# Optimization experiments

Measured on AMD Instinct MI355X. Metric: run time of the kernel, lower is better.

Reference implementation:

```python
import jax, jax.numpy as jnp
import numpy as np

H = 8          # num heads
DK = 64        # d_model // H
D_MODEL = 512
WIN = 256


def setup_inputs() -> dict:
    key = jax.random.key(0)
    ks = jax.random.split(key, 12)
    B, S = 2, 2048
    mk = lambda k, shape, s=1.0: jax.random.normal(k, shape, dtype=jnp.float32) * s
    inp = {
        "query": mk(ks[0], (B, S, D_MODEL)),
        "key_in": mk(ks[1], (B, S, D_MODEL)),
        "value": mk(ks[2], (B, S, D_MODEL)),
        # nn.Linear(d_model, d_model) weights (out,in) and biases, x4
        "Wq": mk(ks[3], (D_MODEL, D_MODEL), 0.02), "bq": jnp.zeros((D_MODEL,), jnp.float32),
        "Wk": mk(ks[4], (D_MODEL, D_MODEL), 0.02), "bk": jnp.zeros((D_MODEL,), jnp.float32),
        "Wv": mk(ks[5], (D_MODEL, D_MODEL), 0.02), "bv": jnp.zeros((D_MODEL,), jnp.float32),
        "Wo": mk(ks[6], (D_MODEL, D_MODEL), 0.02), "bo": jnp.zeros((D_MODEL,), jnp.float32),
    }
    return inp


def reference(query, key_in, value, Wq, bq, Wk, bk, Wv, bv, Wo, bo):
    B, S, D = query.shape
    scale = np.float32(1.0 / np.sqrt(DK))

    def proj(x, W, b):
        # (B,S,D) -> (B,H,S,DK)
        return (x @ W.T + b).reshape(B, S, H, DK).transpose(0, 2, 1, 3)

    q = proj(query, Wq, bq)
    k = proj(key_in, Wk, bk)
    v = proj(value, Wv, bv)

    # Faithful to naive_masked_matmul: full (B,H,S,S) scores, with entries
    # OUTSIDE the sliding window left at exactly 0.0 (NOT -inf) before softmax.
    scores = jnp.einsum('bhid,bhjd->bhij', q, k) * scale
    idx = jnp.arange(S)
    band = jnp.abs(idx[:, None] - idx[None, :]) <= (WIN // 2)  # (S,S) bool
    scores = jnp.where(band, scores, jnp.float32(0.0))

    p_attn = jax.nn.softmax(scores, axis=-1)
    x = jnp.einsum('bhij,bhjd->bhid', p_attn, v)          # (B,H,S,DK)
    x = x.transpose(0, 2, 1, 3).reshape(B, S, D)          # (B,S,D)
    return x @ Wo.T + bo
```

## Files before the change

kernel.cpp:

```cpp
#include <hip/hip_runtime.h>
#include <hip/hip_bf16.h>

#define SS 2048
#define DD 512
#define HWIN 128

typedef __bf16 bf16x8 __attribute__((ext_vector_type(8)));
typedef unsigned short u16x8 __attribute__((ext_vector_type(8)));
typedef float f32x4 __attribute__((ext_vector_type(4)));

__device__ __forceinline__ unsigned short f2bf(float x) {
    unsigned u = __builtin_bit_cast(unsigned, x);
    return (unsigned short)((u + 0x7fffu + ((u >> 16) & 1u)) >> 16);
}
__device__ __forceinline__ float bf2f(unsigned short s) {
    unsigned u = ((unsigned)s) << 16;
    return __builtin_bit_cast(float, u);
}
__device__ __forceinline__ void split_bf(float x, unsigned short& h, unsigned short& l) {
    h = f2bf(x);
    l = f2bf(x - bf2f(h));
}
__device__ __forceinline__ void split8(float4 f0, float4 f1, u16x8& h, u16x8& l) {
    const float vals[8] = {f0.x, f0.y, f0.z, f0.w, f1.x, f1.y, f1.z, f1.w};
    #pragma unroll
    for (int i = 0; i < 8; ++i) {
        unsigned short hh, ll;
        split_bf(vals[i], hh, ll);
        h[i] = hh;
        l[i] = ll;
    }
}
__device__ __forceinline__ f32x4 mfma16(u16x8 a, u16x8 b, f32x4 c) {
    return __builtin_amdgcn_mfma_f32_16x16x32_bf16(
        __builtin_bit_cast(bf16x8, a), __builtin_bit_cast(bf16x8, b), c, 0, 0, 0);
}
__device__ __forceinline__ void gload16(const unsigned short* g, unsigned short* l) {
    __builtin_amdgcn_global_load_lds(
        (const __attribute__((address_space(1))) unsigned int*)g,
        (__attribute__((address_space(3))) unsigned int*)l, 16, 0, 0);
}

__global__ __launch_bounds__(256) void castW(
    const float* __restrict__ wq, const float* __restrict__ wk,
    const float* __restrict__ wv, const float* __restrict__ wo,
    unsigned short* __restrict__ WP, unsigned short* __restrict__ WoP)
{
    const size_t e0 = ((size_t)blockIdx.x * 256 + threadIdx.x) * 8;
    const float* src; size_t off; unsigned short* dst;
    if      (e0 < 262144) { src = wq; off = e0;          dst = WP + 2 * e0; }
    else if (e0 < 524288) { src = wk; off = e0 - 262144; dst = WP + 2 * e0; }
    else if (e0 < 786432) { src = wv; off = e0 - 524288; dst = WP + 2 * e0; }
    else                  { src = wo; off = e0 - 786432; dst = WoP + 2 * (e0 - 786432); }
    u16x8 h, l;
    split8(*(const float4*)(src + off), *(const float4*)(src + off + 4), h, l);
    *(u16x8*)(dst)     = h;
    *(u16x8*)(dst + 8) = l;
}

__global__ __launch_bounds__(256) void proj_gemm(
    const float* __restrict__ q, const float* __restrict__ k, const float* __restrict__ v,
    const unsigned short* __restrict__ WP,
    const float* __restrict__ bq, const float* __restrict__ bk, const float* __restrict__ bv,
    unsigned short* __restrict__ base,
    unsigned short* __restrict__ VTH, unsigned short* __restrict__ VTL)
{
    const int d = blockIdx.x;
    const int hi = d >> 6, low = d & 63;
    const int x = low >> 3, rsw = low & 7;
    const int g = hi * 8 + rsw;
    const int y = g / 3, z = g - y * 3;

    const float* A = (z == 0) ? q : ((z == 1) ? k : v);
    const unsigned short* Wp = WP + (size_t)z * 524288;
    const float* bias = (z == 0) ? bq : ((z == 1) ? bk : bv);
    unsigned short* OH = base + (size_t)z * 4194304;
    unsigned short* OL = OH + 2097152;

    const int m0 = y * 128, n0 = x * 64;

    __shared__ unsigned short Ah[8 * 64 * 8], Al[8 * 64 * 8];
    __shared__ unsigned short Bh[4 * 64 * 8], Bl[4 * 64 * 8];

    const int tid = threadIdx.x, wave = tid >> 6, lane = tid & 63;
    const int lm = lane & 15, lq = lane >> 4;
    const int wm = wave >> 1, wn = wave & 1;
    const int kb = lq * 8;

    f32x4 acc[4][2] = {};

    const int ar0 = m0 + (wave * 2 + 0) * 16 + lm;
    const int ar1 = m0 + (wave * 2 + 1) * 16 + lm;
    const int br  = n0 + wave * 16 + lm;

    unsigned short* aD0h = &Ah[((wave * 2 + 0) * 64 + lane) * 8];
    unsigned short* aD1h = &Ah[((wave * 2 + 1) * 64 + lane) * 8];
    unsigned short* aD0l = &Al[((wave * 2 + 0) * 64 + lane) * 8];
    unsigned short* aD1l = &Al[((wave * 2 + 1) * 64 + lane) * 8];
    unsigned short* bDh  = &Bh[(wave * 64 + lane) * 8];
    unsigned short* bDl  = &Bl[(wave * 64 + lane) * 8];

    for (int k0 = 0; k0 < 512; k0 += 32) {
        const float* p0 = A + (size_t)ar0 * 512 + k0 + kb;
        const float4 f00 = *(const float4*)p0, f01 = *(const float4*)(p0 + 4);
        const float* p1 = A + (size_t)ar1 * 512 + k0 + kb;
        const float4 f10 = *(const float4*)p1, f11 = *(const float4*)(p1 + 4);

        __syncthreads();
        u16x8 a0h, a0l, a1h, a1l;
        split8(f00, f01, a0h, a0l);
        split8(f10, f11, a1h, a1l);
        *(u16x8*)aD0h = a0h; *(u16x8*)aD0l = a0l;
        *(u16x8*)aD1h = a1h; *(u16x8*)aD1l = a1l;
        {
            const unsigned short* pw = Wp + 2 * ((size_t)br * 512 + k0 + kb);
            gload16(pw,     bDh);
            gload16(pw + 8, bDl);
        }
        __syncthreads();

        u16x8 afh[4], afl[4], bfh[2], bfl[2];
        #pragma unroll
        for (int i = 0; i < 4; ++i) {
            afh[i] = *(const u16x8*)&Ah[((wm * 4 + i) * 64 + lane) * 8];
            afl[i] = *(const u16x8*)&Al[((wm * 4 + i) * 64 + lane) * 8];
        }
        #pragma unroll
        for (int j = 0; j < 2; ++j) {
            bfh[j] = *(const u16x8*)&Bh[((wn * 2 + j) * 64 + lane) * 8];
            bfl[j] = *(const u16x8*)&Bl[((wn * 2 + j) * 64 + lane) * 8];
        }
        #pragma unroll
        for (int i = 0; i < 4; ++i)
            #pragma unroll
            for (int j = 0; j < 2; ++j) {
                acc[i][j] = mfma16(afh[i], bfh[j], acc[i][j]);
                acc[i][j] = mfma16(afh[i], bfl[j], acc[i][j]);
                acc[i][j] = mfma16(afl[i], bfh[j], acc[i][j]);
            }
    }

    #pragma unroll
    for (int i = 0; i < 4; ++i)
        #pragma unroll
        for (int j = 0; j < 2; ++j) {
            const int col = n0 + (wn * 2 + j) * 16 + lm;
            const float bv_ = bias[col];
            #pragma unroll
            for (int r = 0; r < 4; ++r) {
                const int row = m0 + (wm * 4 + i) * 16 + lq * 4 + r;
                const float vv = acc[i][j][r] + bv_;
                unsigned short hh, ll;
                split_bf(vv, hh, ll);
                if (z == 2) {
                    const size_t vix =
                        (((size_t)(row >> 11) * 8 + (col >> 6)) * 64 + (col & 63)) * 2048
                        + (row & 2047);
                    VTH[vix] = hh;
                    VTL[vix] = ll;
                } else {
                    OH[(size_t)row * 512 + col] = hh;
                    OL[(size_t)row * 512 + col] = ll;
                }
            }
        }
}

__global__ __launch_bounds__(256) void out_gemm(
    const unsigned short* __restrict__ XHg, const unsigned short* __restrict__ XLg,
    const unsigned short* __restrict__ WoP, const float* __restrict__ bo,
    float* __restrict__ O)
{
    const int gid = blockIdx.x;
    const int rr = gid & 7, hi = gid >> 3;
    const int nblk = hi & 7, mhi = hi >> 3;
    const int mblk = mhi * 8 + rr;
    const int m0 = mblk * 64, n0 = nblk * 64;

    __shared__ unsigned short Ah[4 * 64 * 8], Al[4 * 64 * 8];
    __shared__ unsigned short Bh[4 * 64 * 8], Bl[4 * 64 * 8];

    const int tid = threadIdx.x, wave = tid >> 6, lane = tid & 63;
    const int lm = lane & 15, lq = lane >> 4;
    const int kb = lq * 8;

    f32x4 acc[4] = {};

    const int arow = m0 + wave * 16 + lm;
    unsigned short* aDh = &Ah[(wave * 64 + lane) * 8];
    unsigned short* aDl = &Al[(wave * 64 + lane) * 8];
    unsigned short* bDh = &Bh[(wave * 64 + lane) * 8];
    unsigned short* bDl = &Bl[(wave * 64 + lane) * 8];

    for (int k0 = 0; k0 < 512; k0 += 32) {
        __syncthreads();
        gload16(XHg + (size_t)arow * 512 + k0 + kb, aDh);
        gload16(XLg + (size_t)arow * 512 + k0 + kb, aDl);
        {
            const unsigned short* pw = WoP + 2 * ((size_t)(n0 + wave * 16 + lm) * 512 + k0 + kb);
            gload16(pw,     bDh);
            gload16(pw + 8, bDl);
        }
        __syncthreads();

        const u16x8 a_h = *(const u16x8*)&Ah[(wave * 64 + lane) * 8];
        const u16x8 a_l = *(const u16x8*)&Al[(wave * 64 + lane) * 8];
        #pragma unroll
        for (int j = 0; j < 4; ++j) {
            const u16x8 b_h = *(const u16x8*)&Bh[(j * 64 + lane) * 8];
            const u16x8 b_l = *(const u16x8*)&Bl[(j * 64 + lane) * 8];
            acc[j] = mfma16(a_h, b_h, acc[j]);
            acc[j] = mfma16(a_h, b_l, acc[j]);
            acc[j] = mfma16(a_l, b_h, acc[j]);
        }
    }

    #pragma unroll
    for (int j = 0; j < 4; ++j) {
        const int col = n0 + j * 16 + lm;
        const float bv_ = bo[col];
        #pragma unroll
        for (int r = 0; r < 4; ++r) {
            const int row = m0 + wave * 16 + lq * 4 + r;
            O[(size_t)row * 512 + col] = acc[j][r] + bv_;
        }
    }
}

__global__ __launch_bounds__(256) void vsum_stage1(
    const unsigned short* __restrict__ VTH, const unsigned short* __restrict__ VTL,
    float* __restrict__ partial)
{
    const int bh = blockIdx.x, c = blockIdx.y;
    const int t = threadIdx.x, dd = t & 63, g = t >> 6;
    __shared__ float p[4][64];
    const size_t rb = ((size_t)bh * 64 + dd) * 2048 + c * 64 + g * 16;
    const u16x8 h0 = *(const u16x8*)(VTH + rb), h1 = *(const u16x8*)(VTH + rb + 8);
    const u16x8 l0 = *(const u16x8*)(VTL + rb), l1 = *(const u16x8*)(VTL + rb + 8);
    float acc = 0.f;
    #pragma unroll
    for (int i = 0; i < 8; ++i) acc += bf2f(h0[i]) + bf2f(l0[i]);
    #pragma unroll
    for (int i = 0; i < 8; ++i) acc += bf2f(h1[i]) + bf2f(l1[i]);
    p[g][dd] = acc;
    __syncthreads();
    if (t < 64)
        partial[((size_t)bh * 32 + c) * 64 + t] =
            p[0][t] + p[1][t] + p[2][t] + p[3][t];
}

__global__ __launch_bounds__(64) void vsum_stage2(
    const float* __restrict__ partial, float* __restrict__ VS)
{
    const int bh = blockIdx.x, dd = threadIdx.x;
    float acc = 0.f;
    #pragma unroll 8
    for (int c = 0; c < 32; ++c)
        acc += partial[((size_t)bh * 32 + c) * 64 + dd];
    VS[bh * 64 + dd] = acc;
}

__global__ __launch_bounds__(256) void attn_mfma(
    const unsigned short* __restrict__ QH, const unsigned short* __restrict__ QL,
    const unsigned short* __restrict__ KH, const unsigned short* __restrict__ KL,
    const unsigned short* __restrict__ VTH, const unsigned short* __restrict__ VTL,
    const float* __restrict__ VS,
    unsigned short* __restrict__ XH, unsigned short* __restrict__ XL)
{
    const int dblk = blockIdx.x;
    const int bhi = dblk >> 8, blow = dblk & 255;
    const int xblk = blow >> 3, rrs = blow & 7;
    const int bh = bhi * 8 + rrs;
    const int h = bh & 7, b = bh >> 3;
    const int i0 = xblk * 64;
    const int tid = threadIdx.x, wave = tid >> 6, lane = tid & 63;
    const int lm = lane & 15, lq = lane >> 4;
    const int kb = lq * 8;

    __shared__ unsigned short Kth[64][72], Ktl[64][72];
    __shared__ unsigned short Vth[64][72], Vtl[64][72];
    __shared__ unsigned short Swh[64][72], Swl[64][72];

    const size_t qoff = ((size_t)(b * SS + i0 + wave * 16 + lm)) * DD + h * 64 + kb;
    const u16x8 aQ0h = *(const u16x8*)(QH + qoff);
    const u16x8 aQ0l = *(const u16x8*)(QL + qoff);
    const u16x8 aQ1h = *(const u16x8*)(QH + qoff + 32);
    const u16x8 aQ1l = *(const u16x8*)(QL + qoff + 32);

    f32x4 oacc[4] = {};
    float dacc[4] = {0.f, 0.f, 0.f, 0.f};

    const int sr = tid & 63, sc = (tid >> 6) * 16;

    for (int jt = 0; jt < 5; ++jt) {
        const int jt0 = i0 - 128 + jt * 64;
        {
            const int j = jt0 + sr;
            u16x8 zv = {0,0,0,0,0,0,0,0};
            u16x8 kh0 = zv, kh1 = zv, kl0 = zv, kl1 = zv;
            if (j >= 0 && j < SS) {
                const size_t gb = ((size_t)(b * SS + j)) * DD + h * 64 + sc;
                kh0 = *(const u16x8*)(KH + gb); kh1 = *(const u16x8*)(KH + gb + 8);
                kl0 = *(const u16x8*)(KL + gb); kl1 = *(const u16x8*)(KL + gb + 8);
            }
            *(u16x8*)&Kth[sr][sc]     = kh0; *(u16x8*)&Kth[sr][sc + 8] = kh1;
            *(u16x8*)&Ktl[sr][sc]     = kl0; *(u16x8*)&Ktl[sr][sc + 8] = kl1;

            const int jcol = jt0 + sc;
            u16x8 vh0 = zv, vh1 = zv, vl0 = zv, vl1 = zv;
            if (jcol >= 0 && jcol < SS) {
                const size_t vb = ((size_t)bh * 64 + sr) * 2048 + jcol;
                vh0 = *(const u16x8*)(VTH + vb); vh1 = *(const u16x8*)(VTH + vb + 8);
                vl0 = *(const u16x8*)(VTL + vb); vl1 = *(const u16x8*)(VTL + vb + 8);
            }
            *(u16x8*)&Vth[sr][sc]     = vh0; *(u16x8*)&Vth[sr][sc + 8] = vh1;
            *(u16x8*)&Vtl[sr][sc]     = vl0; *(u16x8*)&Vtl[sr][sc + 8] = vl1;
        }
        __syncthreads();

        #pragma unroll
        for (int js = 0; js < 4; ++js) {
            const int j0 = js * 16;
            const u16x8 bK0h = *(const u16x8*)&Kth[j0 + lm][kb];
            const u16x8 bK0l = *(const u16x8*)&Ktl[j0 + lm][kb];
            const u16x8 bK1h = *(const u16x8*)&Kth[j0 + lm][kb + 32];
            const u16x8 bK1l = *(const u16x8*)&Ktl[j0 + lm][kb + 32];
            f32x4 s = {0.f, 0.f, 0.f, 0.f};
            s = mfma16(aQ0h, bK0h, s);
            s = mfma16(aQ0h, bK0l, s);
            s = mfma16(aQ0l, bK0h, s);
            s = mfma16(aQ1h, bK1h, s);
            s = mfma16(aQ1h, bK1l, s);
            s = mfma16(aQ1l, bK1h, s);
            const int jg = jt0 + j0 + lm;
            const int iq = i0 + wave * 16 + lq * 4;
            #pragma unroll
            for (int r = 0; r < 4; ++r) {
                const int qi = iq + r;
                const bool in = (jg >= 0) && (jg < SS) &&
                                (jg >= qi - HWIN) && (jg <= qi + HWIN);
                const float w = in ? (__expf(s[r] * 0.125f) - 1.0f) : 0.0f;
                dacc[r] += w;
                unsigned short wh, wl;
                split_bf(w, wh, wl);
                Swh[wave * 16 + lq * 4 + r][j0 + lm] = wh;
                Swl[wave * 16 + lq * 4 + r][j0 + lm] = wl;
            }
        }
        __syncthreads();

        const u16x8 aP0h = *(const u16x8*)&Swh[wave * 16 + lm][kb];
        const u16x8 aP0l = *(const u16x8*)&Swl[wave * 16 + lm][kb];
        const u16x8 aP1h = *(const u16x8*)&Swh[wave * 16 + lm][kb + 32];
        const u16x8 aP1l = *(const u16x8*)&Swl[wave * 16 + lm][kb + 32];
        #pragma unroll
        for (int s4 = 0; s4 < 4; ++s4) {
            const u16x8 bV0h = *(const u16x8*)&Vth[s4 * 16 + lm][kb];
            const u16x8 bV0l = *(const u16x8*)&Vtl[s4 * 16 + lm][kb];
            const u16x8 bV1h = *(const u16x8*)&Vth[s4 * 16 + lm][kb + 32];
            const u16x8 bV1l = *(const u16x8*)&Vtl[s4 * 16 + lm][kb + 32];
            oacc[s4] = mfma16(aP0h, bV0h, oacc[s4]);
            oacc[s4] = mfma16(aP0l, bV0h, oacc[s4]);
            oacc[s4] = mfma16(aP0h, bV0l, oacc[s4]);
            oacc[s4] = mfma16(aP1h, bV1h, oacc[s4]);
            oacc[s4] = mfma16(aP1l, bV1h, oacc[s4]);
            oacc[s4] = mfma16(aP1h, bV1l, oacc[s4]);
        }
        __syncthreads();
    }

    #pragma unroll
    for (int r = 0; r < 4; ++r) {
        float v = dacc[r];
        v += __shfl_xor(v, 1);
        v += __shfl_xor(v, 2);
        v += __shfl_xor(v, 4);
        v += __shfl_xor(v, 8);
        dacc[r] = v + 2048.0f;
    }

    #pragma unroll
    for (int s4 = 0; s4 < 4; ++s4) {
        const float vsv = VS[bh * 64 + s4 * 16 + lm];
        #pragma unroll
        for (int r = 0; r < 4; ++r) {
            const int qrow = i0 + wave * 16 + lq * 4 + r;
            const float x = (oacc[s4][r] + vsv) / dacc[r];
            unsigned short xh, xl;
            split_bf(x, xh, xl);
            const size_t ix = ((size_t)(b * SS + qrow)) * DD + h * 64 + s4 * 16 + lm;
            XH[ix] = xh;
            XL[ix] = xl;
        }
    }
}

extern "C" void kernel_launch(void* const* d_in, const int* in_sizes, int n_in,
                              void* d_out, int out_size, void* d_ws, size_t ws_size,
                              hipStream_t stream)
{
    const float* query  = (const float*)d_in[0];
    const float* key_in = (const float*)d_in[1];
    const float* value  = (const float*)d_in[2];
    const float* Wq = (const float*)d_in[3]; const float* bq = (const float*)d_in[4];
    const float* Wk = (const float*)d_in[5]; const float* bk = (const float*)d_in[6];
    const float* Wv = (const float*)d_in[7]; const float* bv = (const float*)d_in[8];
    const float* Wo = (const float*)d_in[9]; const float* bo = (const float*)d_in[10];

    unsigned short* wsb = (unsigned short*)d_ws;
    unsigned short* QH  = wsb;
    unsigned short* QL  = wsb + 2097152;
    unsigned short* KH  = wsb + 4194304;
    unsigned short* KL  = wsb + 6291456;
    unsigned short* VTH = wsb + 8388608;
    unsigned short* VTL = wsb + 10485760;
    unsigned short* XH  = wsb + 12582912;
    unsigned short* XL  = wsb + 14680064;
    unsigned short* WP  = wsb + 16777216;
    unsigned short* WoP = wsb + 18350080;
    float* part = (float*)((char*)d_ws + 62914560);
    float* VSp  = (float*)((char*)d_ws + 63045632);

    castW<<<512, 256, 0, stream>>>(Wq, Wk, Wv, Wo, WP, WoP);

    proj_gemm<<<768, 256, 0, stream>>>(
        query, key_in, value, WP, bq, bk, bv, QH, VTH, VTL);

    vsum_stage1<<<dim3(16, 32), 256, 0, stream>>>(VTH, VTL, part);
    vsum_stage2<<<16, 64, 0, stream>>>(part, VSp);

    attn_mfma<<<512, 256, 0, stream>>>(
        QH, QL, KH, KL, VTH, VTL, VSp, XH, XL);

    out_gemm<<<512, 256, 0, stream>>>(XH, XL, WoP, bo, (float*)d_out);
}
```

Measured before the change: 176.7 us.

## Double K-step in GEMMs and use fragment-ordered LDS with direct global loads in attention

Measured after the change: 178.3 us. About the same (+0.9%).

```diff
diff --git a/kernel.cpp b/kernel.cpp
--- a/kernel.cpp
+++ b/kernel.cpp
@@ -79,8 +79,8 @@
 
     const int m0 = y * 128, n0 = x * 64;
 
-    __shared__ unsigned short Ah[8 * 64 * 8], Al[8 * 64 * 8];
-    __shared__ unsigned short Bh[4 * 64 * 8], Bl[4 * 64 * 8];
+    __shared__ unsigned short Ah[16 * 64 * 8], Al[16 * 64 * 8];
+    __shared__ unsigned short Bh[8 * 64 * 8],  Bl[8 * 64 * 8];
 
     const int tid = threadIdx.x, wave = tid >> 6, lane = tid & 63;
     const int lm = lane & 15, lq = lane >> 4;
@@ -93,51 +93,66 @@
     const int ar1 = m0 + (wave * 2 + 1) * 16 + lm;
     const int br  = n0 + wave * 16 + lm;
 
-    unsigned short* aD0h = &Ah[((wave * 2 + 0) * 64 + lane) * 8];
-    unsigned short* aD1h = &Ah[((wave * 2 + 1) * 64 + lane) * 8];
-    unsigned short* aD0l = &Al[((wave * 2 + 0) * 64 + lane) * 8];
-    unsigned short* aD1l = &Al[((wave * 2 + 1) * 64 + lane) * 8];
-    unsigned short* bDh  = &Bh[(wave * 64 + lane) * 8];
-    unsigned short* bDl  = &Bl[(wave * 64 + lane) * 8];
-
-    for (int k0 = 0; k0 < 512; k0 += 32) {
+    unsigned short* aDh[2][2];
+    unsigned short* aDl[2][2];
+    unsigned short* bDh[2];
+    unsigned short* bDl[2];
+    #pragma unroll
+    for (int s = 0; s < 2; ++s) {
+        aDh[0][s] = &Ah[((s * 8 + wave * 2 + 0) * 64 + lane) * 8];
+        aDh[1][s] = &Ah[((s * 8 + wave * 2 + 1) * 64 + lane) * 8];
+        aDl[0][s] = &Al[((s * 8 + wave * 2 + 0) * 64 + lane) * 8];
+        aDl[1][s] = &Al[((s * 8 + wave * 2 + 1) * 64 + lane) * 8];
+        bDh[s]    = &Bh[((s * 4 + wave) * 64 + lane) * 8];
+        bDl[s]    = &Bl[((s * 4 + wave) * 64 + lane) * 8];
+    }
+
+    for (int k0 = 0; k0 < 512; k0 += 64) {
         const float* p0 = A + (size_t)ar0 * 512 + k0 + kb;
-        const float4 f00 = *(const float4*)p0, f01 = *(const float4*)(p0 + 4);
         const float* p1 = A + (size_t)ar1 * 512 + k0 + kb;
-        const float4 f10 = *(const float4*)p1, f11 = *(const float4*)(p1 + 4);
-
-        __syncthreads();
-        u16x8 a0h, a0l, a1h, a1l;
-        split8(f00, f01, a0h, a0l);
-        split8(f10, f11, a1h, a1l);
-        *(u16x8*)aD0h = a0h; *(u16x8*)aD0l = a0l;
-        *(u16x8*)aD1h = a1h; *(u16x8*)aD1l = a1l;
+        const float4 f000 = *(const float4*)(p0),      f001 = *(const float4*)(p0 + 4);
+        const float4 f010 = *(const float4*)(p0 + 32), f011 = *(const float4*)(p0 + 36);
+        const float4 f100 = *(const float4*)(p1),      f101 = *(const float4*)(p1 + 4);
+        const float4 f110 = *(const float4*)(p1 + 32), f111 = *(const float4*)(p1 + 36);
+
+        __syncthreads();
         {
-            const unsigned short* pw = Wp + 2 * ((size_t)br * 512 + k0 + kb);
-            gload16(pw,     bDh);
-            gload16(pw + 8, bDl);
-        }
-        __syncthreads();
-
-        u16x8 afh[4], afl[4], bfh[2], bfl[2];
-        #pragma unroll
-        for (int i = 0; i < 4; ++i) {
-            afh[i] = *(const u16x8*)&Ah[((wm * 4 + i) * 64 + lane) * 8];
-            afl[i] = *(const u16x8*)&Al[((wm * 4 + i) * 64 + lane) * 8];
-        }
-        #pragma unroll
-        for (int j = 0; j < 2; ++j) {
-            bfh[j] = *(const u16x8*)&Bh[((wn * 2 + j) * 64 + lane) * 8];
-            bfl[j] = *(const u16x8*)&Bl[((wn * 2 + j) * 64 + lane) * 8];
-        }
-        #pragma unroll
-        for (int i = 0; i < 4; ++i)
+            u16x8 hh, ll;
+            split8(f000, f001, hh, ll); *(u16x8*)aDh[0][0] = hh; *(u16x8*)aDl[0][0] = ll;
+            split8(f010, f011, hh, ll); *(u16x8*)aDh[0][1] = hh; *(u16x8*)aDl[0][1] = ll;
+            split8(f100, f101, hh, ll); *(u16x8*)aDh[1][0] = hh; *(u16x8*)aDl[1][0] = ll;
+            split8(f110, f111, hh, ll); *(u16x8*)aDh[1][1] = hh; *(u16x8*)aDl[1][1] = ll;
+        }
+        #pragma unroll
+        for (int s = 0; s < 2; ++s) {
+            const unsigned short* pw = Wp + 2 * ((size_t)br * 512 + k0 + s * 32 + kb);
+            gload16(pw,     bDh[s]);
+            gload16(pw + 8, bDl[s]);
+        }
+        __syncthreads();
+
+        #pragma unroll
+        for (int s = 0; s < 2; ++s) {
+            u16x8 afh[4], afl[4], bfh[2], bfl[2];
+            #pragma unroll
+            for (int i = 0; i < 4; ++i) {
+                afh[i] = *(const u16x8*)&Ah[((s * 8 + wm * 4 + i) * 64 + lane) * 8];
+                afl[i] = *(const u16x8*)&Al[((s * 8 + wm * 4 + i) * 64 + lane) * 8];
+            }
             #pragma unroll
             for (int j = 0; j < 2; ++j) {
-                acc[i][j] = mfma16(afh[i], bfh[j], acc[i][j]);
-                acc[i][j] = mfma16(afh[i], bfl[j], acc[i][j]);
-                acc[i][j] = mfma16(afl[i], bfh[j], acc[i][j]);
+                bfh[j] = *(const u16x8*)&Bh[((s * 4 + wn * 2 + j) * 64 + lane) * 8];
+                bfl[j] = *(const u16x8*)&Bl[((s * 4 + wn * 2 + j) * 64 + lane) * 8];
             }
+            #pragma unroll
+            for (int i = 0; i < 4; ++i)
+                #pragma unroll
+                for (int j = 0; j < 2; ++j) {
+                    acc[i][j] = mfma16(afh[i], bfh[j], acc[i][j]);
+                    acc[i][j] = mfma16(afh[i], bfl[j], acc[i][j]);
+                    acc[i][j] = mfma16(afl[i], bfh[j], acc[i][j]);
+                }
+        }
     }
 
     #pragma unroll
@@ -177,8 +192,8 @@
     const int mblk = mhi * 8 + rr;
     const int m0 = mblk * 64, n0 = nblk * 64;
 
-    __shared__ unsigned short Ah[4 * 64 * 8], Al[4 * 64 * 8];
-    __shared__ unsigned short Bh[4 * 64 * 8], Bl[4 * 64 * 8];
+    __shared__ unsigned short Ah[8 * 64 * 8], Al[8 * 64 * 8];
+    __shared__ unsigned short Bh[8 * 64 * 8], Bl[8 * 64 * 8];
 
     const int tid = threadIdx.x, wave = tid >> 6, lane = tid & 63;
     const int lm = lane & 15, lq = lane >> 4;
@@ -187,31 +202,34 @@
     f32x4 acc[4] = {};
 
     const int arow = m0 + wave * 16 + lm;
-    unsigned short* aDh = &Ah[(wave * 64 + lane) * 8];
-    unsigned short* aDl = &Al[(wave * 64 + lane) * 8];
-    unsigned short* bDh = &Bh[(wave * 64 + lane) * 8];
-    unsigned short* bDl = &Bl[(wave * 64 + lane) * 8];
-
-    for (int k0 = 0; k0 < 512; k0 += 32) {
-        __syncthreads();
-        gload16(XHg + (size_t)arow * 512 + k0 + kb, aDh);
-        gload16(XLg + (size_t)arow * 512 + k0 + kb, aDl);
-        {
-            const unsigned short* pw = WoP + 2 * ((size_t)(n0 + wave * 16 + lm) * 512 + k0 + kb);
-            gload16(pw,     bDh);
-            gload16(pw + 8, bDl);
-        }
-        __syncthreads();
-
-        const u16x8 a_h = *(const u16x8*)&Ah[(wave * 64 + lane) * 8];
-        const u16x8 a_l = *(const u16x8*)&Al[(wave * 64 + lane) * 8];
-        #pragma unroll
-        for (int j = 0; j < 4; ++j) {
-            const u16x8 b_h = *(const u16x8*)&Bh[(j * 64 + lane) * 8];
-            const u16x8 b_l = *(const u16x8*)&Bl[(j * 64 + lane) * 8];
-            acc[j] = mfma16(a_h, b_h, acc[j]);
-            acc[j] = mfma16(a_h, b_l, acc[j]);
-            acc[j] = mfma16(a_l, b_h, acc[j]);
+    const int brow = n0 + wave * 16 + lm;
+
+    for (int k0 = 0; k0 < 512; k0 += 64) {
+        __syncthreads();
+        #pragma unroll
+        for (int s = 0; s < 2; ++s) {
+            gload16(XHg + (size_t)arow * 512 + k0 + s * 32 + kb,
+                    &Ah[((s * 4 + wave) * 64 + lane) * 8]);
+            gload16(XLg + (size_t)arow * 512 + k0 + s * 32 + kb,
+                    &Al[((s * 4 + wave) * 64 + lane) * 8]);
+            const unsigned short* pw = WoP + 2 * ((size_t)brow * 512 + k0 + s * 32 + kb);
+            gload16(pw,     &Bh[((s * 4 + wave) * 64 + lane) * 8]);
+            gload16(pw + 8, &Bl[((s * 4 + wave) * 64 + lane) * 8]);
+        }
+        __syncthreads();
+
+        #pragma unroll
+        for (int s = 0; s < 2; ++s) {
+            const u16x8 a_h = *(const u16x8*)&Ah[((s * 4 + wave) * 64 + lane) * 8];
+            const u16x8 a_l = *(const u16x8*)&Al[((s * 4 + wave) * 64 + lane) * 8];
+            #pragma unroll
+            for (int j = 0; j < 4; ++j) {
+                const u16x8 b_h = *(const u16x8*)&Bh[((s * 4 + j) * 64 + lane) * 8];
+                const u16x8 b_l = *(const u16x8*)&Bl[((s * 4 + j) * 64 + lane) * 8];
+                acc[j] = mfma16(a_h, b_h, acc[j]);
+                acc[j] = mfma16(a_h, b_l, acc[j]);
+                acc[j] = mfma16(a_l, b_h, acc[j]);
+            }
         }
     }
 
@@ -277,8 +295,8 @@
     const int lm = lane & 15, lq = lane >> 4;
     const int kb = lq * 8;
 
-    __shared__ unsigned short Kth[64][72], Ktl[64][72];
-    __shared__ unsigned short Vth[64][72], Vtl[64][72];
+    __shared__ unsigned short KfH[8 * 64 * 8], KfL[8 * 64 * 8];
+    __shared__ unsigned short VfH[8 * 64 * 8], VfL[8 * 64 * 8];
     __shared__ unsigned short Swh[64][72], Swl[64][72];
 
     const size_t qoff = ((size_t)(b * SS + i0 + wave * 16 + lm)) * DD + h * 64 + kb;
@@ -290,41 +308,42 @@
     f32x4 oacc[4] = {};
     float dacc[4] = {0.f, 0.f, 0.f, 0.f};
 
-    const int sr = tid & 63, sc = (tid >> 6) * 16;
+    unsigned short* kDh0 = &KfH[((wave * 2 + 0) * 64 + lane) * 8];
+    unsigned short* kDh1 = &KfH[((wave * 2 + 1) * 64 + lane) * 8];
+    unsigned short* kDl0 = &KfL[((wave * 2 + 0) * 64 + lane) * 8];
+    unsigned short* kDl1 = &KfL[((wave * 2 + 1) * 64 + lane) * 8];
+    unsigned short* vDh0 = &VfH[((wave * 2 + 0) * 64 + lane) * 8];
+    unsigned short* vDh1 = &VfH[((wave * 2 + 1) * 64 + lane) * 8];
+    unsigned short* vDl0 = &VfL[((wave * 2 + 0) * 64 + lane) * 8];
+    unsigned short* vDl1 = &VfL[((wave * 2 + 1) * 64 + lane) * 8];
+    const size_t vrow = ((size_t)bh * 64 + wave * 16 + lm) * 2048;
 
     for (int jt = 0; jt < 5; ++jt) {
         const int jt0 = i0 - 128 + jt * 64;
         {
-            const int j = jt0 + sr;
-            u16x8 zv = {0,0,0,0,0,0,0,0};
-            u16x8 kh0 = zv, kh1 = zv, kl0 = zv, kl1 = zv;
-            if (j >= 0 && j < SS) {
-                const size_t gb = ((size_t)(b * SS + j)) * DD + h * 64 + sc;
-                kh0 = *(const u16x8*)(KH + gb); kh1 = *(const u16x8*)(KH + gb + 8);
-                kl0 = *(const u16x8*)(KL + gb); kl1 = *(const u16x8*)(KL + gb + 8);
-            }
-            *(u16x8*)&Kth[sr][sc]     = kh0; *(u16x8*)&Kth[sr][sc + 8] = kh1;
-            *(u16x8*)&Ktl[sr][sc]     = kl0; *(u16x8*)&Ktl[sr][sc + 8] = kl1;
-
-            const int jcol = jt0 + sc;
-            u16x8 vh0 = zv, vh1 = zv, vl0 = zv, vl1 = zv;
-            if (jcol >= 0 && jcol < SS) {
-                const size_t vb = ((size_t)bh * 64 + sr) * 2048 + jcol;
-                vh0 = *(const u16x8*)(VTH + vb); vh1 = *(const u16x8*)(VTH + vb + 8);
-                vl0 = *(const u16x8*)(VTL + vb); vl1 = *(const u16x8*)(VTL + vb + 8);
-            }
-            *(u16x8*)&Vth[sr][sc]     = vh0; *(u16x8*)&Vth[sr][sc + 8] = vh1;
-            *(u16x8*)&Vtl[sr][sc]     = vl0; *(u16x8*)&Vtl[sr][sc + 8] = vl1;
+            const int jrow = jt0 + wave * 16 + lm;
+            const int jrc = min(max(jrow, 0), SS - 1);
+            const size_t kgb = ((size_t)(b * SS + jrc)) * DD + h * 64 + kb;
+            gload16(KH + kgb,      kDh0);
+            gload16(KH + kgb + 32, kDh1);
+            gload16(KL + kgb,      kDl0);
+            gload16(KL + kgb + 32, kDl1);
+            const int j0c = min(max(jt0 + kb, 0), SS - 8);
+            const int j1c = min(max(jt0 + 32 + kb, 0), SS - 8);
+            gload16(VTH + vrow + j0c, vDh0);
+            gload16(VTH + vrow + j1c, vDh1);
+            gload16(VTL + vrow + j0c, vDl0);
+            gload16(VTL + vrow + j1c, vDl1);
         }
         __syncthreads();
 
         #pragma unroll
         for (int js = 0; js < 4; ++js) {
             const int j0 = js * 16;
-            const u16x8 bK0h = *(const u16x8*)&Kth[j0 + lm][kb];
-            const u16x8 bK0l = *(const u16x8*)&Ktl[j0 + lm][kb];
-            const u16x8 bK1h = *(const u16x8*)&Kth[j0 + lm][kb + 32];
-            const u16x8 bK1l = *(const u16x8*)&Ktl[j0 + lm][kb + 32];
+            const u16x8 bK0h = *(const u16x8*)&KfH[((js * 2 + 0) * 64 + lane) * 8];
+            const u16x8 bK0l = *(const u16x8*)&KfL[((js * 2 + 0) * 64 + lane) * 8];
+            const u16x8 bK1h = *(const u16x8*)&KfH[((js * 2 + 1) * 64 + lane) * 8];
+            const u16x8 bK1l = *(const u16x8*)&KfL[((js * 2 + 1) * 64 + lane) * 8];
             f32x4 s = {0.f, 0.f, 0.f, 0.f};
             s = mfma16(aQ0h, bK0h, s);
             s = mfma16(aQ0h, bK0l, s);
@@ -355,10 +374,10 @@
         const u16x8 aP1l = *(const u16x8*)&Swl[wave * 16 + lm][kb + 32];
         #pragma unroll
         for (int s4 = 0; s4 < 4; ++s4) {
-            const u16x8 bV0h = *(const u16x8*)&Vth[s4 * 16 + lm][kb];
-            const u16x8 bV0l = *(const u16x8*)&Vtl[s4 * 16 + lm][kb];
-            const u16x8 bV1h = *(const u16x8*)&Vth[s4 * 16 + lm][kb + 32];
-            const u16x8 bV1l = *(const u16x8*)&Vtl[s4 * 16 + lm][kb + 32];
+            const u16x8 bV0h = *(const u16x8*)&VfH[((s4 * 2 + 0) * 64 + lane) * 8];
+            const u16x8 bV0l = *(const u16x8*)&VfL[((s4 * 2 + 0) * 64 + lane) * 8];
+            const u16x8 bV1h = *(const u16x8*)&VfH[((s4 * 2 + 1) * 64 + lane) * 8];
+            const u16x8 bV1l = *(const u16x8*)&VfL[((s4 * 2 + 1) * 64 + lane) * 8];
             oacc[s4] = mfma16(aP0h, bV0h, oacc[s4]);
             oacc[s4] = mfma16(aP0l, bV0h, oacc[s4]);
             oacc[s4] = mfma16(aP0h, bV0l, oacc[s4]);
```
